# Performance work log

Hardware: AMD Instinct MI355X
Metric: run time of the kernel (lower is better)

Reference implementation:

```python
import jax, jax.numpy as jnp
import numpy as np

N, E = 10000, 160000
D_IN, H, L = 128, 256, 3


def setup_inputs() -> dict:
    key = jax.random.key(0)
    ks = jax.random.split(key, 16)

    def lin(k, fan_in, fan_out):
        return jax.random.normal(k, (fan_in, fan_out), jnp.float32) / np.sqrt(fan_in)

    inp = {
        "node_feats": jax.random.normal(ks[0], (N, D_IN), jnp.float32),
        "gh": jax.random.normal(ks[1], (E, H), jnp.float32),
        "src": jax.random.randint(ks[2], (E,), 0, N),
        "dst": jax.random.randint(ks[3], (E,), 0, N),
        # W_n: Linear(node_in_feats, H)
        "W_n_w": lin(ks[4], D_IN, H),
        "W_n_b": jnp.zeros((H,), jnp.float32),
        # per-layer eps MLP: Linear(H,H) -> ReLU -> Linear(H,1)
        "eps_w1": jnp.stack([lin(jax.random.fold_in(ks[5], l), H, H) for l in range(L)]),
        "eps_b1": jnp.zeros((L, H), jnp.float32),
        "eps_w2": jnp.stack([lin(jax.random.fold_in(ks[6], l), H, 1) for l in range(L)]),
        "eps_b2": jnp.zeros((L, 1), jnp.float32),
        # per-layer attention MLP: Linear(3H,H) -> ReLU -> Linear(H,1)  (pretrain=True -> dim=3)
        "a_w1": jnp.stack([lin(jax.random.fold_in(ks[7], l), 3 * H, H) for l in range(L)]),
        "a_b1": jnp.zeros((L, H), jnp.float32),
        "a_w2": jnp.stack([lin(jax.random.fold_in(ks[8], l), H, 1) for l in range(L)]),
        "a_b2": jnp.zeros((L, 1), jnp.float32),
    }
    return inp


def reference(node_feats, gh, src, dst, W_n_w, W_n_b,
              eps_w1, eps_b1, eps_w2, eps_b2,
              a_w1, a_b1, a_w2, a_b2):
    n = node_feats.shape[0]
    # input projection (dropout is identity in eval)
    h = node_feats @ W_n_w + W_n_b  # [N, H]
    outs = [h]
    n_layers = eps_w1.shape[0]
    for l in range(n_layers):
        # per-edge attention score: MLP(concat(h_src, h_dst, gh)) -> [E, 1]
        cat = jnp.concatenate([h[src], h[dst], gh], axis=-1)  # [E, 3H]
        a = jax.nn.relu(cat @ a_w1[l] + a_b1[l]) @ a_w2[l] + a_b2[l]  # [E, 1]
        # edge_softmax over incoming edges of each destination node
        amax = jax.ops.segment_max(a, dst, num_segments=n)  # [N, 1]
        ea = jnp.exp(a - amax[dst])
        denom = jax.ops.segment_sum(ea, dst, num_segments=n)  # [N, 1]
        att = ea / denom[dst]  # [E, 1]
        # message: a * (h_src * gh), scatter-sum into dst
        m = att * (h[src] * gh)  # [E, H]
        hv = jax.ops.segment_sum(m, dst, num_segments=n)  # [N, H]
        # GIN-style update with learned per-node epsilon scalar
        eps = jax.nn.relu(h @ eps_w1[l] + eps_b1[l]) @ eps_w2[l] + eps_b2[l]  # [N, 1]
        h = (1.0 + eps) * hv + h
        outs.append(h)
    return tuple(outs)
```

## Files before the change

### kernel.cpp

```cpp
#include <hip/hip_runtime.h>
#include <hip/hip_bf16.h>
#include <math.h>

#define D_INF 128
#define HF    256
#define LF    3

typedef float f32x4 __attribute__((ext_vector_type(4)));
typedef short bf16x8 __attribute__((ext_vector_type(8)));

__device__ inline void rne_bf16(float x, short& h, float& hf) {
    uint32_t u = __float_as_uint(x);
    uint32_t r = u + 0x7FFFu + ((u >> 16) & 1u);
    r &= 0xFFFF0000u;
    h = (short)(r >> 16);
    hf = __uint_as_float(r);
}

__global__ __launch_bounds__(256) void gemm_f32(
    const float* __restrict__ A, const float* __restrict__ B,
    const float* __restrict__ bias, float* __restrict__ C,
    int M, int K, int N)
{
    __shared__ __align__(16) float As[16][68];
    __shared__ __align__(16) float Bs[16][68];
    const int tid = threadIdx.x;
    const int tx = tid & 15, ty = tid >> 4;
    const int row0 = blockIdx.x * 64;
    const int col0 = blockIdx.y * 64;
    float acc[4][4] = {};

    for (int k0 = 0; k0 < K; k0 += 16) {
        {
            int m = tid >> 2, kk4 = (tid & 3) << 2;
            int gr = row0 + m;
            float4 v = make_float4(0.f, 0.f, 0.f, 0.f);
            if (gr < M) v = *(const float4*)(A + (size_t)gr * K + k0 + kk4);
            As[kk4 + 0][m] = v.x;
            As[kk4 + 1][m] = v.y;
            As[kk4 + 2][m] = v.z;
            As[kk4 + 3][m] = v.w;
        }
        {
            int kk = tid >> 4, n4 = (tid & 15) << 2;
            float4 v = *(const float4*)(B + (size_t)(k0 + kk) * N + col0 + n4);
            *(float4*)&Bs[kk][n4] = v;
        }
        __syncthreads();
        #pragma unroll
        for (int kk = 0; kk < 16; kk++) {
            float a4[4], b4[4];
            *(float4*)a4 = *(const float4*)&As[kk][ty << 2];
            *(float4*)b4 = *(const float4*)&Bs[kk][tx << 2];
            #pragma unroll
            for (int i = 0; i < 4; i++)
                #pragma unroll
                for (int j = 0; j < 4; j++)
                    acc[i][j] += a4[i] * b4[j];
        }
        __syncthreads();
    }

    int c = col0 + (tx << 2);
    #pragma unroll
    for (int i = 0; i < 4; i++) {
        int r = row0 + (ty << 2) + i;
        if (r >= M) continue;
        float4 o;
        o.x = acc[i][0]; o.y = acc[i][1]; o.z = acc[i][2]; o.w = acc[i][3];
        if (bias) {
            o.x += bias[c + 0]; o.y += bias[c + 1];
            o.z += bias[c + 2]; o.w += bias[c + 3];
        }
        *(float4*)(C + (size_t)r * N + c) = o;
    }
}

__global__ __launch_bounds__(256) void mlp_score_kernel(
    const float* __restrict__ A, const float* __restrict__ B,
    const float* __restrict__ b1, const float* __restrict__ w2,
    const float* __restrict__ b2,
    const float* __restrict__ P1, const float* __restrict__ P2,
    const int* __restrict__ src, const int* __restrict__ dst,
    float* __restrict__ out, int M, int K)
{
    __shared__ __align__(16) float As[16][68];
    __shared__ __align__(16) float Bs[16][260];
    const int tid = threadIdx.x;
    const int tx = tid & 15, ty = tid >> 4;
    const int row0 = blockIdx.x * 64;
    float acc[4][16] = {};

    for (int k0 = 0; k0 < K; k0 += 16) {
        {
            int m = tid >> 2, kk4 = (tid & 3) << 2;
            int gr = row0 + m;
            float4 v = make_float4(0.f, 0.f, 0.f, 0.f);
            if (gr < M) v = *(const float4*)(A + (size_t)gr * K + k0 + kk4);
            As[kk4 + 0][m] = v.x;
            As[kk4 + 1][m] = v.y;
            As[kk4 + 2][m] = v.z;
            As[kk4 + 3][m] = v.w;
        }
        {
            int kk = ty;
            int cb = tx << 4;
            const float* bp = B + (size_t)(k0 + kk) * HF + cb;
            *(float4*)&Bs[kk][cb +  0] = *(const float4*)(bp +  0);
            *(float4*)&Bs[kk][cb +  4] = *(const float4*)(bp +  4);
            *(float4*)&Bs[kk][cb +  8] = *(const float4*)(bp +  8);
            *(float4*)&Bs[kk][cb + 12] = *(const float4*)(bp + 12);
        }
        __syncthreads();
        #pragma unroll
        for (int kk = 0; kk < 16; kk++) {
            float a4[4];
            *(float4*)a4 = *(const float4*)&As[kk][ty << 2];
            float b16[16];
            #pragma unroll
            for (int cb = 0; cb < 4; cb++)
                *(float4*)&b16[cb * 4] = *(const float4*)&Bs[kk][cb * 64 + (tx << 2)];
            #pragma unroll
            for (int i = 0; i < 4; i++)
                #pragma unroll
                for (int j = 0; j < 16; j++)
                    acc[i][j] += a4[i] * b16[j];
        }
        __syncthreads();
    }

    float b1v[16], w2v[16];
    #pragma unroll
    for (int cb = 0; cb < 4; cb++) {
        *(float4*)&b1v[cb * 4] = *(const float4*)(b1 + cb * 64 + (tx << 2));
        *(float4*)&w2v[cb * 4] = *(const float4*)(w2 + cb * 64 + (tx << 2));
    }
    const float bias2 = b2[0];

    #pragma unroll
    for (int i = 0; i < 4; i++) {
        int r = row0 + (ty << 2) + i;
        if (r < M) {
            float p = 0.f;
            if (P1) {
                const float* p1 = P1 + (size_t)src[r] * HF;
                const float* p2 = P2 + (size_t)dst[r] * HF;
                #pragma unroll
                for (int cb = 0; cb < 4; cb++) {
                    float g1[4], g2[4];
                    *(float4*)g1 = *(const float4*)(p1 + cb * 64 + (tx << 2));
                    *(float4*)g2 = *(const float4*)(p2 + cb * 64 + (tx << 2));
                    #pragma unroll
                    for (int j = 0; j < 4; j++) {
                        float v = acc[i][cb * 4 + j] + g1[j] + g2[j] + b1v[cb * 4 + j];
                        p += fmaxf(v, 0.f) * w2v[cb * 4 + j];
                    }
                }
            } else {
                #pragma unroll
                for (int j = 0; j < 16; j++) {
                    float v = acc[i][j] + b1v[j];
                    p += fmaxf(v, 0.f) * w2v[j];
                }
            }
            #pragma unroll
            for (int o = 8; o > 0; o >>= 1) p += __shfl_down(p, o, 16);
            if (tx == 0) out[r] = p + bias2;
        }
    }
}

__global__ void conv_w1cT_kernel(const float* __restrict__ a_w1,
                                 short* __restrict__ WhiT, short* __restrict__ WloT)
{
    int t = blockIdx.x * blockDim.x + threadIdx.x;
    if (t >= LF * HF * HF) return;
    int c  = t & 255;
    int k  = (t >> 8) & 255;
    int ly = t >> 16;
    float x = a_w1[((size_t)ly * 3 * HF + 2 * HF + k) * HF + c];
    short hh, ll; float hf, lf_;
    rne_bf16(x, hh, hf);
    rne_bf16(x - hf, ll, lf_);
    int ck = k >> 5;
    int j  = ((((k >> 3) & 3) ^ ((c >> 2) & 3)) << 3) + (k & 7);
    size_t d = (((size_t)ly * 8 + ck) * 256 + c) * 32 + j;
    WhiT[d] = hh;
    WloT[d] = ll;
}

__global__ __launch_bounds__(256) void edge_mfma_kernel(
    const float* __restrict__ gh,
    const short* __restrict__ WhiT, const short* __restrict__ WloT,
    const float* __restrict__ b1, const float* __restrict__ w2,
    const float* __restrict__ b2,
    const float* __restrict__ P1, const float* __restrict__ P2,
    const int* __restrict__ src, const int* __restrict__ dst,
    float* __restrict__ out)
{
    __shared__ __align__(16) short Ahi[64 * 32];
    __shared__ __align__(16) short Alo[64 * 32];
    __shared__ __align__(16) short Bhi[256 * 32];
    __shared__ __align__(16) short Blo[256 * 32];
    __shared__ float part[64][4];

    const int tid = threadIdx.x;
    const int w   = tid >> 6;
    const int l   = tid & 63;
    const int g   = l >> 4;
    const int e0  = blockIdx.x * 64;

    const f32x4 zero4 = {0.f, 0.f, 0.f, 0.f};
    f32x4 acc[4][4];
    #pragma unroll
    for (int i = 0; i < 4; i++)
        #pragma unroll
        for (int j = 0; j < 4; j++)
            acc[i][j] = zero4;

    for (int ck = 0; ck < 8; ck++) {
        const int k0 = ck * 32;
        {
            const short* sHi = WhiT + (size_t)ck * (256 * 32);
            const short* sLo = WloT + (size_t)ck * (256 * 32);
            #pragma unroll
            for (int p = 0; p < 4; p++) {
                int off8 = (p * 256 + tid) * 8;
                *(bf16x8*)&Bhi[off8] = *(const bf16x8*)&sHi[off8];
                *(bf16x8*)&Blo[off8] = *(const bf16x8*)&sLo[off8];
            }
        }
        {
            const int r = tid >> 2, p = tid & 3;
            const float* gp = gh + (size_t)(e0 + r) * HF + k0 + p * 8;
            float vf[8];
            *(float4*)&vf[0] = *(const float4*)gp;
            *(float4*)&vf[4] = *(const float4*)(gp + 4);
            bf16x8 hv, lv;
            #pragma unroll
            for (int j = 0; j < 8; j++) {
                short hh, ll; float hf, lf_;
                rne_bf16(vf[j], hh, hf);
                rne_bf16(vf[j] - hf, ll, lf_);
                hv[j] = hh;
                lv[j] = ll;
            }
            const int s = p ^ ((r >> 2) & 3);
            *(bf16x8*)&Ahi[(r * 4 + s) * 8] = hv;
            *(bf16x8*)&Alo[(r * 4 + s) * 8] = lv;
        }
        __syncthreads();

        bf16x8 ah[4], al[4];
        #pragma unroll
        for (int rt = 0; rt < 4; rt++) {
            int r = rt * 16 + (l & 15);
            int s = g ^ ((r >> 2) & 3);
            ah[rt] = *(const bf16x8*)&Ahi[(r * 4 + s) * 8];
            al[rt] = *(const bf16x8*)&Alo[(r * 4 + s) * 8];
        }
        #pragma unroll
        for (int ct = 0; ct < 4; ct++) {
            int c = w * 64 + ct * 16 + (l & 15);
            int s = g ^ ((c >> 2) & 3);
            bf16x8 bh = *(const bf16x8*)&Bhi[(c * 4 + s) * 8];
            bf16x8 bl = *(const bf16x8*)&Blo[(c * 4 + s) * 8];
            #pragma unroll
            for (int rt = 0; rt < 4; rt++) {
                acc[rt][ct] = __builtin_amdgcn_mfma_f32_16x16x32_bf16(ah[rt], bh, acc[rt][ct], 0, 0, 0);
                acc[rt][ct] = __builtin_amdgcn_mfma_f32_16x16x32_bf16(al[rt], bh, acc[rt][ct], 0, 0, 0);
                acc[rt][ct] = __builtin_amdgcn_mfma_f32_16x16x32_bf16(ah[rt], bl, acc[rt][ct], 0, 0, 0);
            }
        }
        __syncthreads();
    }

    float w2v[4], b1v[4];
    #pragma unroll
    for (int ct = 0; ct < 4; ct++) {
        int c = w * 64 + ct * 16 + (l & 15);
        w2v[ct] = w2[c];
        b1v[ct] = b1[c];
    }
    #pragma unroll
    for (int rt = 0; rt < 4; rt++) {
        #pragma unroll
        for (int i = 0; i < 4; i++) {
            int r = rt * 16 + g * 4 + i;
            int e = e0 + r;
            const float* p1 = P1 + (size_t)src[e] * HF;
            const float* p2 = P2 + (size_t)dst[e] * HF;
            float p = 0.f;
            #pragma unroll
            for (int ct = 0; ct < 4; ct++) {
                int c = w * 64 + ct * 16 + (l & 15);
                float v = acc[rt][ct][i] + p1[c] + p2[c] + b1v[ct];
                p += fmaxf(v, 0.f) * w2v[ct];
            }
            #pragma unroll
            for (int o = 8; o > 0; o >>= 1) p += __shfl_down(p, o, 16);
            if ((l & 15) == 0) part[r][w] = p;
        }
    }
    __syncthreads();
    if (tid < 64)
        out[e0 + tid] = part[tid][0] + part[tid][1] + part[tid][2] + part[tid][3] + b2[0];
}

__global__ void hist_kernel(const int* __restrict__ dst, int* __restrict__ deg, int E)
{
    int e = blockIdx.x * blockDim.x + threadIdx.x;
    if (e < E) atomicAdd(&deg[dst[e]], 1);
}

__global__ __launch_bounds__(1024) void scan_kernel(
    const int* __restrict__ deg, int* __restrict__ off, int* __restrict__ cur, int n)
{
    __shared__ int sums[1024];
    const int tid = threadIdx.x;
    const int chunk = (n + 1023) / 1024;
    const int start = tid * chunk;
    const int end = (start + chunk < n) ? (start + chunk) : n;
    int s = 0;
    for (int i = start; i < end; i++) s += deg[i];
    sums[tid] = s;
    __syncthreads();
    for (int d = 1; d < 1024; d <<= 1) {
        int t = 0;
        if (tid >= d) t = sums[tid - d];
        __syncthreads();
        if (tid >= d) sums[tid] += t;
        __syncthreads();
    }
    int run = (tid > 0) ? sums[tid - 1] : 0;
    for (int i = start; i < end; i++) {
        off[i] = run;
        cur[i] = run;
        run += deg[i];
    }
    if (tid == 1023) off[n] = sums[1023];
}

__global__ void fill_kernel(const int* __restrict__ dst, int* __restrict__ cur,
                            int* __restrict__ el, int E)
{
    int e = blockIdx.x * blockDim.x + threadIdx.x;
    if (e < E) {
        int p = atomicAdd(&cur[dst[e]], 1);
        el[p] = e;
    }
}

__global__ __launch_bounds__(256) void node_agg_update_kernel(
    const float* __restrict__ a, const int* __restrict__ off,
    const int* __restrict__ el, const int* __restrict__ src,
    const float* __restrict__ h, const float* __restrict__ gh,
    const float* __restrict__ eps, float* __restrict__ hn, int N)
{
    const int node = blockIdx.x * 4 + (threadIdx.x >> 6);
    const int lane = threadIdx.x & 63;
    if (node >= N) return;
    const int beg = off[node];
    const int deg = off[node + 1] - beg;
    const int c4 = lane << 2;

    float4 acc = make_float4(0.f, 0.f, 0.f, 0.f);
    if (deg > 0) {
        float mx = -INFINITY;
        for (int i = lane; i < deg; i += 64) mx = fmaxf(mx, a[el[beg + i]]);
        #pragma unroll
        for (int o = 32; o > 0; o >>= 1) mx = fmaxf(mx, __shfl_xor(mx, o, 64));
        float sm = 0.f;
        for (int i = lane; i < deg; i += 64) sm += expf(a[el[beg + i]] - mx);
        #pragma unroll
        for (int o = 32; o > 0; o >>= 1) sm += __shfl_xor(sm, o, 64);
        const float inv = 1.f / sm;
        for (int i = 0; i < deg; i++) {
            const int e = el[beg + i];
            const float at = expf(a[e] - mx) * inv;
            const float4 hs = *(const float4*)(h + (size_t)src[e] * HF + c4);
            const float4 ge = *(const float4*)(gh + (size_t)e * HF + c4);
            acc.x += at * hs.x * ge.x;
            acc.y += at * hs.y * ge.y;
            acc.z += at * hs.z * ge.z;
            acc.w += at * hs.w * ge.w;
        }
    }
    const float s = 1.f + eps[node];
    const float4 hp = *(const float4*)(h + (size_t)node * HF + c4);
    float4 o;
    o.x = s * acc.x + hp.x;
    o.y = s * acc.y + hp.y;
    o.z = s * acc.z + hp.z;
    o.w = s * acc.w + hp.w;
    *(float4*)(hn + (size_t)node * HF + c4) = o;
}

extern "C" void kernel_launch(void* const* d_in, const int* in_sizes, int n_in,
                              void* d_out, int out_size, void* d_ws, size_t ws_size,
                              hipStream_t stream)
{
    const float* node_feats = (const float*)d_in[0];
    const float* gh     = (const float*)d_in[1];
    const int*   src    = (const int*)d_in[2];
    const int*   dst    = (const int*)d_in[3];
    const float* Wn_w   = (const float*)d_in[4];
    const float* Wn_b   = (const float*)d_in[5];
    const float* eps_w1 = (const float*)d_in[6];
    const float* eps_b1 = (const float*)d_in[7];
    const float* eps_w2 = (const float*)d_in[8];
    const float* eps_b2 = (const float*)d_in[9];
    const float* a_w1   = (const float*)d_in[10];
    const float* a_b1   = (const float*)d_in[11];
    const float* a_w2   = (const float*)d_in[12];
    const float* a_b2   = (const float*)d_in[13];
    float* out = (float*)d_out;

    const int N = in_sizes[0] / D_INF;
    const int E = in_sizes[2];

    char* ws = (char*)d_ws;
    size_t off = 0;
    auto carve = [&](size_t bytes) -> void* {
        void* p = ws + off;
        off = (off + bytes + 255) & ~(size_t)255;
        return p;
    };
    float* P1  = (float*)carve((size_t)N * HF * 4);
    float* P2  = (float*)carve((size_t)N * HF * 4);
    float* ASC = (float*)carve((size_t)E * 4);
    float* EPS = (float*)carve((size_t)N * 4);
    int*   DEG = (int*)carve((size_t)N * 4);
    int*   OFFS= (int*)carve((size_t)(N + 1) * 4);
    int*   CUR = (int*)carve((size_t)N * 4);
    int*   EL  = (int*)carve((size_t)E * 4);
    short* WhiT= (short*)carve((size_t)LF * HF * HF * 2);
    short* WloT= (short*)carve((size_t)LF * HF * HF * 2);
    const bool use_mfma = (off <= ws_size) && (E % 64 == 0);

    hipMemsetAsync(DEG, 0, (size_t)N * 4, stream);
    hist_kernel<<<(E + 255) / 256, 256, 0, stream>>>(dst, DEG, E);
    scan_kernel<<<1, 1024, 0, stream>>>(DEG, OFFS, CUR, N);
    fill_kernel<<<(E + 255) / 256, 256, 0, stream>>>(dst, CUR, EL, E);

    if (use_mfma)
        conv_w1cT_kernel<<<(LF * HF * HF + 255) / 256, 256, 0, stream>>>(a_w1, WhiT, WloT);

    dim3 gg((N + 63) / 64, HF / 64);

    gemm_f32<<<gg, 256, 0, stream>>>(node_feats, Wn_w, Wn_b, out, N, D_INF, HF);

    const int egrid = (E + 63) / 64;
    const int ngrid = (N + 63) / 64;

    for (int l = 0; l < LF; l++) {
        const float* h  = out + (size_t)l * N * HF;
        float*       hn = out + (size_t)(l + 1) * N * HF;
        const float* W1  = a_w1 + (size_t)l * 3 * HF * HF;
        const float* W1a = W1;
        const float* W1b = W1 + (size_t)HF * HF;
        const float* W1c = W1 + (size_t)2 * HF * HF;
        const float* b1  = a_b1 + (size_t)l * HF;
        const float* w2  = a_w2 + (size_t)l * HF;
        const float* b2  = a_b2 + l;

        gemm_f32<<<gg, 256, 0, stream>>>(h, W1a, nullptr, P1, N, HF, HF);
        gemm_f32<<<gg, 256, 0, stream>>>(h, W1b, nullptr, P2, N, HF, HF);

        if (use_mfma) {
            edge_mfma_kernel<<<E / 64, 256, 0, stream>>>(
                gh, WhiT + (size_t)l * HF * HF, WloT + (size_t)l * HF * HF,
                b1, w2, b2, P1, P2, src, dst, ASC);
        } else {
            mlp_score_kernel<<<egrid, 256, 0, stream>>>(
                gh, W1c, b1, w2, b2, P1, P2, src, dst, ASC, E, HF);
        }

        mlp_score_kernel<<<ngrid, 256, 0, stream>>>(
            h, eps_w1 + (size_t)l * HF * HF, eps_b1 + (size_t)l * HF,
            eps_w2 + (size_t)l * HF, eps_b2 + l,
            nullptr, nullptr, nullptr, nullptr, EPS, N, HF);

        node_agg_update_kernel<<<(N + 3) / 4, 256, 0, stream>>>(
            ASC, OFFS, EL, src, h, gh, EPS, hn, N);
    }
}
```

Baseline: 1.135 ms.

## Move node GEMMs to split-bf16 MFMA with blocked layouts and async LDS pipeline

Pre-splits gh, node features, per-layer h and all weights into hi/lo bf16 pairs stored in a 64-row blocked layout. All GEMMs (input projection, P1/P2, eps MLP, edge score) then run on 3-pass bf16 MFMA, with operands staged by global_load_lds into double-buffered LDS. The P1, P2 and eps GEMMs are fused into one launch that uses a grid y-dimension, replacing several fp32 SIMT GEMM launches. In exchange it adds conversion passes and a large workspace for the split gh copy, and falls back to the old path if the workspace is too small.

```diff
diff --git a/kernel.cpp b/kernel.cpp
--- a/kernel.cpp
+++ b/kernel.cpp
@@ -9,12 +9,18 @@
 typedef float f32x4 __attribute__((ext_vector_type(4)));
 typedef short bf16x8 __attribute__((ext_vector_type(8)));
 
-__device__ inline void rne_bf16(float x, short& h, float& hf) {
+__device__ __forceinline__ void rne_bf16(float x, short& h, float& hf) {
     uint32_t u = __float_as_uint(x);
     uint32_t r = u + 0x7FFFu + ((u >> 16) & 1u);
     r &= 0xFFFF0000u;
     h = (short)(r >> 16);
     hf = __uint_as_float(r);
+}
+
+__device__ __forceinline__ void glds16(const void* g, void* l) {
+    __builtin_amdgcn_global_load_lds(
+        (const __attribute__((address_space(1))) void*)g,
+        (__attribute__((address_space(3))) void*)l, 16, 0, 0);
 }
 
 __global__ __launch_bounds__(256) void gemm_f32(
@@ -210,13 +216,12 @@
     const int g   = l >> 4;
     const int e0  = blockIdx.x * 64;
 
-    const f32x4 zero4 = {0.f, 0.f, 0.f, 0.f};
     f32x4 acc[4][4];
     #pragma unroll
     for (int i = 0; i < 4; i++)
         #pragma unroll
         for (int j = 0; j < 4; j++)
-            acc[i][j] = zero4;
+            acc[i][j] = (f32x4){0.f, 0.f, 0.f, 0.f};
 
     for (int ck = 0; ck < 8; ck++) {
         const int k0 = ck * 32;
@@ -305,6 +310,338 @@
     __syncthreads();
     if (tid < 64)
         out[e0 + tid] = part[tid][0] + part[tid][1] + part[tid][2] + part[tid][3] + b2[0];
+}
+
+
+__global__ void split_blocked_kernel(const float* __restrict__ x,
+                                     short* __restrict__ hi, short* __restrict__ lo,
+                                     long M, int K, int kgshift)
+{
+    const long n8 = M << kgshift;
+    const int kgmask = (1 << kgshift) - 1;
+    for (long i = (long)blockIdx.x * blockDim.x + threadIdx.x; i < n8;
+         i += (long)gridDim.x * blockDim.x) {
+        long e = i >> kgshift;
+        int k0 = (int)(i & kgmask) << 3;
+        const float* p = x + e * K + k0;
+        float v[8];
+        *(float4*)&v[0] = *(const float4*)p;
+        *(float4*)&v[4] = *(const float4*)(p + 4);
+        bf16x8 h8, l8;
+        #pragma unroll
+        for (int j = 0; j < 8; j++) {
+            short hh, ll; float hf, lf_;
+            rne_bf16(v[j], hh, hf);
+            rne_bf16(v[j] - hf, ll, lf_);
+            h8[j] = hh; l8[j] = ll;
+        }
+        size_t d = (size_t)(e >> 6) * ((size_t)K << 6) + (size_t)(k0 >> 5) * 2048
+                 + (size_t)(e & 63) * 32 + (k0 & 31);
+        *(bf16x8*)&hi[d] = h8;
+        *(bf16x8*)&lo[d] = l8;
+    }
+}
+
+__global__ void conv_aw1_kernel(const float* __restrict__ a_w1,
+                                short* __restrict__ Whi, short* __restrict__ Wlo)
+{
+    int t = blockIdx.x * blockDim.x + threadIdx.x;
+    if (t >= LF * 3 * HF * HF) return;
+    int c = t & 255;
+    int k = (t >> 8) & 255;
+    int b = (t >> 16) % 3;
+    int l = t / (3 * HF * HF);
+    float x = a_w1[((size_t)l * 3 * HF + b * HF + k) * HF + c];
+    short hh, ll; float hf, lf_;
+    rne_bf16(x, hh, hf);
+    rne_bf16(x - hf, ll, lf_);
+    size_t d = (size_t)(l * 3 + b) * 65536 + (size_t)(k >> 5) * 8192 + c * 32 + (k & 31);
+    Whi[d] = hh;
+    Wlo[d] = ll;
+}
+
+__global__ void conv_epsw1_kernel(const float* __restrict__ eps_w1,
+                                  short* __restrict__ Ehi, short* __restrict__ Elo)
+{
+    int t = blockIdx.x * blockDim.x + threadIdx.x;
+    if (t >= LF * HF * HF) return;
+    int c = t & 255;
+    int k = (t >> 8) & 255;
+    int l = t >> 16;
+    float x = eps_w1[((size_t)l * HF + k) * HF + c];
+    short hh, ll; float hf, lf_;
+    rne_bf16(x, hh, hf);
+    rne_bf16(x - hf, ll, lf_);
+    size_t d = (size_t)l * 65536 + (size_t)(k >> 5) * 8192 + c * 32 + (k & 31);
+    Ehi[d] = hh;
+    Elo[d] = ll;
+}
+
+__global__ void conv_wn_kernel(const float* __restrict__ Wn,
+                               short* __restrict__ Whi, short* __restrict__ Wlo)
+{
+    int t = blockIdx.x * blockDim.x + threadIdx.x;
+    if (t >= D_INF * HF) return;
+    int c = t & 255;
+    int k = t >> 8;
+    float x = Wn[(size_t)k * HF + c];
+    short hh, ll; float hf, lf_;
+    rne_bf16(x, hh, hf);
+    rne_bf16(x - hf, ll, lf_);
+    size_t d = (size_t)(k >> 5) * 8192 + c * 32 + (k & 31);
+    Whi[d] = hh;
+    Wlo[d] = ll;
+}
+
+#define LDSB 40960
+
+__device__ __forceinline__ void stage_ab(
+    char* sb,
+    const short* __restrict__ Ah, const short* __restrict__ Al,
+    const short* __restrict__ Bh, const short* __restrict__ Bl,
+    int w, int l)
+{
+    const int a_off = w * 512 + l * 8;
+    glds16(Ah + a_off, sb + w * 1024);
+    glds16(Al + a_off, sb + 4096 + w * 1024);
+    const int loff = l * 8;
+    #pragma unroll
+    for (int i = 0; i < 4; i++) {
+        int q = (w << 2) + i;
+        glds16(Bh + q * 512 + loff, sb + 8192  + q * 1024);
+        glds16(Bl + q * 512 + loff, sb + 24576 + q * 1024);
+    }
+}
+
+__device__ __forceinline__ void compute_chunk(
+    const char* cb, int w, int lr, int g, f32x4 acc[4][4])
+{
+    const short* Ah = (const short*)(cb);
+    const short* Al = (const short*)(cb + 4096);
+    const short* Bh = (const short*)(cb + 8192);
+    const short* Bl = (const short*)(cb + 24576);
+    bf16x8 ah[4], al[4];
+    #pragma unroll
+    for (int rt = 0; rt < 4; rt++) {
+        int r = rt * 16 + lr;
+        ah[rt] = *(const bf16x8*)&Ah[r * 32 + g * 8];
+        al[rt] = *(const bf16x8*)&Al[r * 32 + g * 8];
+    }
+    #pragma unroll
+    for (int ct = 0; ct < 4; ct++) {
+        int c = w * 64 + ct * 16 + lr;
+        bf16x8 bh = *(const bf16x8*)&Bh[c * 32 + g * 8];
+        bf16x8 bl = *(const bf16x8*)&Bl[c * 32 + g * 8];
+        #pragma unroll
+        for (int rt = 0; rt < 4; rt++) {
+            acc[rt][ct] = __builtin_amdgcn_mfma_f32_16x16x32_bf16(ah[rt], bh, acc[rt][ct], 0, 0, 0);
+            acc[rt][ct] = __builtin_amdgcn_mfma_f32_16x16x32_bf16(al[rt], bh, acc[rt][ct], 0, 0, 0);
+            acc[rt][ct] = __builtin_amdgcn_mfma_f32_16x16x32_bf16(ah[rt], bl, acc[rt][ct], 0, 0, 0);
+        }
+    }
+}
+
+__global__ __launch_bounds__(256) void edge_mfma2_kernel(
+    const short* __restrict__ ghhi, const short* __restrict__ ghlo,
+    const short* __restrict__ Wc_hi, const short* __restrict__ Wc_lo,
+    const float* __restrict__ b1, const float* __restrict__ w2,
+    const float* __restrict__ b2,
+    const float* __restrict__ P1, const float* __restrict__ P2,
+    const int* __restrict__ src, const int* __restrict__ dst,
+    float* __restrict__ out)
+{
+    __shared__ __align__(16) char smem[2 * LDSB];
+    const int tid = threadIdx.x;
+    const int w = tid >> 6, l = tid & 63;
+    const int lr = l & 15, g = l >> 4;
+    const long row0 = (long)blockIdx.x * 64;
+    const size_t ablk = (size_t)blockIdx.x << 14;
+
+    f32x4 acc[4][4];
+    #pragma unroll
+    for (int i = 0; i < 4; i++)
+        #pragma unroll
+        for (int j = 0; j < 4; j++)
+            acc[i][j] = (f32x4){0.f, 0.f, 0.f, 0.f};
+
+    stage_ab(smem, ghhi + ablk, ghlo + ablk, Wc_hi, Wc_lo, w, l);
+    __syncthreads();
+    for (int ck = 0; ck < 8; ck++) {
+        if (ck < 7)
+            stage_ab(smem + ((ck + 1) & 1) * LDSB,
+                     ghhi + ablk + (ck + 1) * 2048, ghlo + ablk + (ck + 1) * 2048,
+                     Wc_hi + (ck + 1) * 8192, Wc_lo + (ck + 1) * 8192, w, l);
+        compute_chunk(smem + (ck & 1) * LDSB, w, lr, g, acc);
+        __syncthreads();
+    }
+
+    float* part = (float*)smem;
+    float w2v[4], b1v[4];
+    #pragma unroll
+    for (int ct = 0; ct < 4; ct++) {
+        int c = w * 64 + ct * 16 + lr;
+        w2v[ct] = w2[c];
+        b1v[ct] = b1[c];
+    }
+    #pragma unroll
+    for (int rt = 0; rt < 4; rt++) {
+        #pragma unroll
+        for (int i = 0; i < 4; i++) {
+            int r = rt * 16 + g * 4 + i;
+            long e = row0 + r;
+            const float* p1 = P1 + (size_t)src[e] * HF;
+            const float* p2 = P2 + (size_t)dst[e] * HF;
+            float p = 0.f;
+            #pragma unroll
+            for (int ct = 0; ct < 4; ct++) {
+                int c = w * 64 + ct * 16 + lr;
+                float v = acc[rt][ct][i] + p1[c] + p2[c] + b1v[ct];
+                p += fmaxf(v, 0.f) * w2v[ct];
+            }
+            #pragma unroll
+            for (int o = 8; o > 0; o >>= 1) p += __shfl_down(p, o, 16);
+            if (lr == 0) part[r * 4 + w] = p;
+        }
+    }
+    __syncthreads();
+    if (tid < 64)
+        out[row0 + tid] = part[tid * 4 + 0] + part[tid * 4 + 1] +
+                          part[tid * 4 + 2] + part[tid * 4 + 3] + b2[0];
+}
+
+__global__ __launch_bounds__(256) void node_mfma_kernel(
+    const short* __restrict__ hhi, const short* __restrict__ hlo,
+    const short* __restrict__ Wa_hi, const short* __restrict__ Wa_lo,
+    const short* __restrict__ Ee_hi, const short* __restrict__ Ee_lo,
+    const float* __restrict__ eb1, const float* __restrict__ ew2,
+    const float* __restrict__ eb2,
+    float* __restrict__ P1o, float* __restrict__ P2o,
+    float* __restrict__ EPSo, int N)
+{
+    __shared__ __align__(16) char smem[2 * LDSB];
+    const int tid = threadIdx.x;
+    const int w = tid >> 6, l = tid & 63;
+    const int lr = l & 15, g = l >> 4;
+    const int y = blockIdx.y;
+    const long row0 = (long)blockIdx.x * 64;
+    const size_t ablk = (size_t)blockIdx.x << 14;
+
+    const short* Bhi_g;
+    const short* Blo_g;
+    if (y == 0)      { Bhi_g = Wa_hi;         Blo_g = Wa_lo; }
+    else if (y == 1) { Bhi_g = Wa_hi + 65536; Blo_g = Wa_lo + 65536; }
+    else             { Bhi_g = Ee_hi;         Blo_g = Ee_lo; }
+
+    f32x4 acc[4][4];
+    #pragma unroll
+    for (int i = 0; i < 4; i++)
+        #pragma unroll
+        for (int j = 0; j < 4; j++)
+            acc[i][j] = (f32x4){0.f, 0.f, 0.f, 0.f};
+
+    stage_ab(smem, hhi + ablk, hlo + ablk, Bhi_g, Blo_g, w, l);
+    __syncthreads();
+    for (int ck = 0; ck < 8; ck++) {
+        if (ck < 7)
+            stage_ab(smem + ((ck + 1) & 1) * LDSB,
+                     hhi + ablk + (ck + 1) * 2048, hlo + ablk + (ck + 1) * 2048,
+                     Bhi_g + (ck + 1) * 8192, Blo_g + (ck + 1) * 8192, w, l);
+        compute_chunk(smem + (ck & 1) * LDSB, w, lr, g, acc);
+        __syncthreads();
+    }
+
+    if (y < 2) {
+        float* P = (y == 0) ? P1o : P2o;
+        #pragma unroll
+        for (int rt = 0; rt < 4; rt++) {
+            #pragma unroll
+            for (int i = 0; i < 4; i++) {
+                long grow = row0 + rt * 16 + g * 4 + i;
+                if (grow < N) {
+                    #pragma unroll
+                    for (int ct = 0; ct < 4; ct++) {
+                        int c = w * 64 + ct * 16 + lr;
+                        P[grow * HF + c] = acc[rt][ct][i];
+                    }
+                }
+            }
+        }
+    } else {
+        float* part = (float*)smem;
+        float w2v[4], b1v[4];
+        #pragma unroll
+        for (int ct = 0; ct < 4; ct++) {
+            int c = w * 64 + ct * 16 + lr;
+            w2v[ct] = ew2[c];
+            b1v[ct] = eb1[c];
+        }
+        #pragma unroll
+        for (int rt = 0; rt < 4; rt++) {
+            #pragma unroll
+            for (int i = 0; i < 4; i++) {
+                int r = rt * 16 + g * 4 + i;
+                float p = 0.f;
+                #pragma unroll
+                for (int ct = 0; ct < 4; ct++) {
+                    float v = acc[rt][ct][i] + b1v[ct];
+                    p += fmaxf(v, 0.f) * w2v[ct];
+                }
+                #pragma unroll
+                for (int o = 8; o > 0; o >>= 1) p += __shfl_down(p, o, 16);
+                if (lr == 0) part[r * 4 + w] = p;
+            }
+        }
+        __syncthreads();
+        if (tid < 64 && row0 + tid < N)
+            EPSo[row0 + tid] = part[tid * 4 + 0] + part[tid * 4 + 1] +
+                               part[tid * 4 + 2] + part[tid * 4 + 3] + eb2[0];
+    }
+}
+
+__global__ __launch_bounds__(256) void proj_mfma_kernel(
+    const short* __restrict__ nfhi, const short* __restrict__ nflo,
+    const short* __restrict__ Wnhi, const short* __restrict__ Wnlo,
+    const float* __restrict__ bias, float* __restrict__ out, int N)
+{
+    __shared__ __align__(16) char smem[2 * LDSB];
+    const int tid = threadIdx.x;
+    const int w = tid >> 6, l = tid & 63;
+    const int lr = l & 15, g = l >> 4;
+    const long row0 = (long)blockIdx.x * 64;
+    const size_t ablk = (size_t)blockIdx.x << 13;
+
+    f32x4 acc[4][4];
+    #pragma unroll
+    for (int i = 0; i < 4; i++)
+        #pragma unroll
+        for (int j = 0; j < 4; j++)
+            acc[i][j] = (f32x4){0.f, 0.f, 0.f, 0.f};
+
+    stage_ab(smem, nfhi + ablk, nflo + ablk, Wnhi, Wnlo, w, l);
+    __syncthreads();
+    for (int ck = 0; ck < 4; ck++) {
+        if (ck < 3)
+            stage_ab(smem + ((ck + 1) & 1) * LDSB,
+                     nfhi + ablk + (ck + 1) * 2048, nflo + ablk + (ck + 1) * 2048,
+                     Wnhi + (ck + 1) * 8192, Wnlo + (ck + 1) * 8192, w, l);
+        compute_chunk(smem + (ck & 1) * LDSB, w, lr, g, acc);
+        __syncthreads();
+    }
+
+    #pragma unroll
+    for (int rt = 0; rt < 4; rt++) {
+        #pragma unroll
+        for (int i = 0; i < 4; i++) {
+            long grow = row0 + rt * 16 + g * 4 + i;
+            if (grow < N) {
+                #pragma unroll
+                for (int ct = 0; ct < 4; ct++) {
+                    int c = w * 64 + ct * 16 + lr;
+                    out[grow * HF + c] = acc[rt][ct][i] + bias[c];
+                }
+            }
+        }
+    }
 }
 
 __global__ void hist_kernel(const int* __restrict__ dst, int* __restrict__ deg, int E)
@@ -418,6 +755,8 @@
 
     const int N = in_sizes[0] / D_INF;
     const int E = in_sizes[2];
+    const int NP64 = ((N + 63) / 64) * 64;
+    const int nblk = NP64 / 64;
 
     char* ws = (char*)d_ws;
     size_t off = 0;
@@ -434,54 +773,107 @@
     int*   OFFS= (int*)carve((size_t)(N + 1) * 4);
     int*   CUR = (int*)carve((size_t)N * 4);
     int*   EL  = (int*)carve((size_t)E * 4);
-    short* WhiT= (short*)carve((size_t)LF * HF * HF * 2);
-    short* WloT= (short*)carve((size_t)LF * HF * HF * 2);
-    const bool use_mfma = (off <= ws_size) && (E % 64 == 0);
+    const size_t common_end = off;
+    short* GHH = (short*)carve((size_t)E * HF * 2);
+    short* GHL = (short*)carve((size_t)E * HF * 2);
+    short* HHI = (short*)carve((size_t)NP64 * HF * 2);
+    short* HLO = (short*)carve((size_t)NP64 * HF * 2);
+    short* NFH = (short*)carve((size_t)NP64 * D_INF * 2);
+    short* NFL = (short*)carve((size_t)NP64 * D_INF * 2);
+    short* WHI = (short*)carve((size_t)LF * 3 * HF * HF * 2);
+    short* WLO = (short*)carve((size_t)LF * 3 * HF * HF * 2);
+    short* EHI = (short*)carve((size_t)LF * HF * HF * 2);
+    short* ELO = (short*)carve((size_t)LF * HF * HF * 2);
+    short* WNH = (short*)carve((size_t)D_INF * HF * 2);
+    short* WNL = (short*)carve((size_t)D_INF * HF * 2);
+    const bool fast = (off <= ws_size) && (E % 64 == 0);
 
     hipMemsetAsync(DEG, 0, (size_t)N * 4, stream);
     hist_kernel<<<(E + 255) / 256, 256, 0, stream>>>(dst, DEG, E);
     scan_kernel<<<1, 1024, 0, stream>>>(DEG, OFFS, CUR, N);
     fill_kernel<<<(E + 255) / 256, 256, 0, stream>>>(dst, CUR, EL, E);
 
-    if (use_mfma)
-        conv_w1cT_kernel<<<(LF * HF * HF + 255) / 256, 256, 0, stream>>>(a_w1, WhiT, WloT);
-
-    dim3 gg((N + 63) / 64, HF / 64);
-
-    gemm_f32<<<gg, 256, 0, stream>>>(node_feats, Wn_w, Wn_b, out, N, D_INF, HF);
-
-    const int egrid = (E + 63) / 64;
-    const int ngrid = (N + 63) / 64;
-
-    for (int l = 0; l < LF; l++) {
-        const float* h  = out + (size_t)l * N * HF;
-        float*       hn = out + (size_t)(l + 1) * N * HF;
-        const float* W1  = a_w1 + (size_t)l * 3 * HF * HF;
-        const float* W1a = W1;
-        const float* W1b = W1 + (size_t)HF * HF;
-        const float* W1c = W1 + (size_t)2 * HF * HF;
-        const float* b1  = a_b1 + (size_t)l * HF;
-        const float* w2  = a_w2 + (size_t)l * HF;
-        const float* b2  = a_b2 + l;
-
-        gemm_f32<<<gg, 256, 0, stream>>>(h, W1a, nullptr, P1, N, HF, HF);
-        gemm_f32<<<gg, 256, 0, stream>>>(h, W1b, nullptr, P2, N, HF, HF);
-
-        if (use_mfma) {
-            edge_mfma_kernel<<<E / 64, 256, 0, stream>>>(
-                gh, WhiT + (size_t)l * HF * HF, WloT + (size_t)l * HF * HF,
+    if (fast) {
+        conv_aw1_kernel<<<(LF * 3 * HF * HF + 255) / 256, 256, 0, stream>>>(a_w1, WHI, WLO);
+        conv_epsw1_kernel<<<(LF * HF * HF + 255) / 256, 256, 0, stream>>>(eps_w1, EHI, ELO);
+        conv_wn_kernel<<<(D_INF * HF + 255) / 256, 256, 0, stream>>>(Wn_w, WNH, WNL);
+        split_blocked_kernel<<<512, 256, 0, stream>>>(node_feats, NFH, NFL, N, D_INF, 4);
+        split_blocked_kernel<<<2048, 256, 0, stream>>>(gh, GHH, GHL, E, HF, 5);
+
+        proj_mfma_kernel<<<nblk, 256, 0, stream>>>(NFH, NFL, WNH, WNL, Wn_b, out, N);
+
+        for (int l = 0; l < LF; l++) {
+            const float* h  = out + (size_t)l * N * HF;
+            float*       hn = out + (size_t)(l + 1) * N * HF;
+            const float* b1 = a_b1 + (size_t)l * HF;
+            const float* w2 = a_w2 + (size_t)l * HF;
+            const float* b2 = a_b2 + l;
+
+            split_blocked_kernel<<<1024, 256, 0, stream>>>(h, HHI, HLO, N, HF, 5);
+
+            node_mfma_kernel<<<dim3(nblk, 3), 256, 0, stream>>>(
+                HHI, HLO,
+                WHI + (size_t)l * 3 * 65536, WLO + (size_t)l * 3 * 65536,
+                EHI + (size_t)l * 65536, ELO + (size_t)l * 65536,
+                eps_b1 + (size_t)l * HF, eps_w2 + (size_t)l * HF, eps_b2 + l,
+                P1, P2, EPS, N);
+
+            edge_mfma2_kernel<<<E / 64, 256, 0, stream>>>(
+                GHH, GHL,
+                WHI + (size_t)(l * 3 + 2) * 65536, WLO + (size_t)(l * 3 + 2) * 65536,
                 b1, w2, b2, P1, P2, src, dst, ASC);
-        } else {
-            mlp_score_kernel<<<egrid, 256, 0, stream>>>(
-                gh, W1c, b1, w2, b2, P1, P2, src, dst, ASC, E, HF);
-        }
-
-        mlp_score_kernel<<<ngrid, 256, 0, stream>>>(
-            h, eps_w1 + (size_t)l * HF * HF, eps_b1 + (size_t)l * HF,
-            eps_w2 + (size_t)l * HF, eps_b2 + l,
-            nullptr, nullptr, nullptr, nullptr, EPS, N, HF);
-
-        node_agg_update_kernel<<<(N + 3) / 4, 256, 0, stream>>>(
-            ASC, OFFS, EL, src, h, gh, EPS, hn, N);
-    }
-}
+
+            node_agg_update_kernel<<<(N + 3) / 4, 256, 0, stream>>>(
+                ASC, OFFS, EL, src, h, gh, EPS, hn, N);
+        }
+    } else {
+        size_t foff = common_end;
+        auto fcarve = [&](size_t bytes) -> void* {
+            void* p = ws + foff;
+            foff = (foff + bytes + 255) & ~(size_t)255;
+            return p;
+        };
+        short* WhiT = (short*)fcarve((size_t)LF * HF * HF * 2);
+        short* WloT = (short*)fcarve((size_t)LF * HF * HF * 2);
+        const bool mf = (foff <= ws_size) && (E % 64 == 0);
+        if (mf)
+            conv_w1cT_kernel<<<(LF * HF * HF + 255) / 256, 256, 0, stream>>>(a_w1, WhiT, WloT);
+
+        dim3 gg((N + 63) / 64, HF / 64);
+        gemm_f32<<<gg, 256, 0, stream>>>(node_feats, Wn_w, Wn_b, out, N, D_INF, HF);
+
+        const int egrid = (E + 63) / 64;
+        const int ngrid = (N + 63) / 64;
+        for (int l = 0; l < LF; l++) {
+            const float* h  = out + (size_t)l * N * HF;
+            float*       hn = out + (size_t)(l + 1) * N * HF;
+            const float* W1  = a_w1 + (size_t)l * 3 * HF * HF;
+            const float* W1a = W1;
+            const float* W1b = W1 + (size_t)HF * HF;
+            const float* W1c = W1 + (size_t)2 * HF * HF;
+            const float* b1  = a_b1 + (size_t)l * HF;
+            const float* w2  = a_w2 + (size_t)l * HF;
+            const float* b2  = a_b2 + l;
+
+            gemm_f32<<<gg, 256, 0, stream>>>(h, W1a, nullptr, P1, N, HF, HF);
+            gemm_f32<<<gg, 256, 0, stream>>>(h, W1b, nullptr, P2, N, HF, HF);
+
+            if (mf) {
+                edge_mfma_kernel<<<E / 64, 256, 0, stream>>>(
+                    gh, WhiT + (size_t)l * HF * HF, WloT + (size_t)l * HF * HF,
+                    b1, w2, b2, P1, P2, src, dst, ASC);
+            } else {
+                mlp_score_kernel<<<egrid, 256, 0, stream>>>(
+                    gh, W1c, b1, w2, b2, P1, P2, src, dst, ASC, E, HF);
+            }
+
+            mlp_score_kernel<<<ngrid, 256, 0, stream>>>(
+                h, eps_w1 + (size_t)l * HF * HF, eps_b1 + (size_t)l * HF,
+                eps_w2 + (size_t)l * HF, eps_b2 + l,
+                nullptr, nullptr, nullptr, nullptr, EPS, N, HF);
+
+            node_agg_update_kernel<<<(N + 3) / 4, 256, 0, stream>>>(
+                ASC, OFFS, EL, src, h, gh, EPS, hn, N);
+        }
+    }
+}
```

New measurement: 1.018 ms. 1.11x faster.
